# Kernel optimization log

Hardware: AMD Instinct MI355X
Metric: run time of the kernel (lower is better)

The kernel has to match this reference:

```python
import jax, jax.numpy as jnp
import numpy as np

N_NODES = 50000
N_EDGES = 262144
HID = 256
N_CLS = 2


def setup_inputs() -> dict:
    key = jax.random.key(0)
    ks = jax.random.split(key, 6)
    node_repr = jax.random.normal(ks[0], (N_NODES, HID), dtype=jnp.float32)
    src = jax.random.randint(ks[1], (N_EDGES,), 0, N_NODES, dtype=jnp.int64)
    dst = jax.random.randint(ks[2], (N_EDGES,), 0, N_NODES, dtype=jnp.int64)
    # Linear weights stored as (in, out); init ~ torch default scale
    W1 = jax.random.normal(ks[3], (4 * HID, 2 * HID), dtype=jnp.float32) * (1.0 / np.sqrt(4 * HID))
    b1 = jnp.zeros((2 * HID,), dtype=jnp.float32)
    W2 = jax.random.normal(ks[4], (2 * HID, N_CLS), dtype=jnp.float32) * (1.0 / np.sqrt(2 * HID))
    b2 = jnp.zeros((N_CLS,), dtype=jnp.float32)
    return {"node_repr": node_repr, "src": src, "dst": dst,
            "W1": W1, "b1": b1, "W2": W2, "b2": b2}


def reference(node_repr, src, dst, W1, b1, W2, b2):
    h_i = node_repr[src]                      # [E, H] gather
    h_j = node_repr[dst]                      # [E, H] gather
    edge_input = jnp.concatenate(
        [h_i, h_j, jnp.abs(h_i - h_j), h_i * h_j], axis=1)  # [E, 4H]
    h = jax.nn.relu(edge_input @ W1 + b1)     # [E, 2H]; dropout = identity (eval)
    return h @ W2 + b2                        # [E, C]
```

## Files before the change

### kernel.cpp

```cpp
#include <hip/hip_runtime.h>

#define N_NODES 50000
#define E_EDGES 262144

typedef __attribute__((ext_vector_type(8))) _Float16 f16x8;
typedef __attribute__((ext_vector_type(2))) _Float16 f16x2;
typedef __attribute__((ext_vector_type(4))) float f32x4;

union V16 { uint4 u; f16x8 h; };
union U32 { unsigned u; f16x2 p; };

__device__ __forceinline__ unsigned h2pack(float a, float b) {
  union { _Float16 h[2]; unsigned u; } r;
  r.h[0] = (_Float16)a;
  r.h[1] = (_Float16)b;
  return r.u;
}
__device__ __forceinline__ void async_gather16(const void* gptr, void* lptr) {
  __builtin_amdgcn_global_load_lds(
      (const __attribute__((address_space(1))) void*)gptr,
      (__attribute__((address_space(3))) void*)lptr, 16, 0, 0);
}

__global__ __launch_bounds__(256) void prep_all_kernel(
    const float* __restrict__ node, const float* __restrict__ w1,
    unsigned short* __restrict__ nodeb, unsigned short* __restrict__ w1pp2) {
  const int bx = blockIdx.x;
  if (bx < 6250) {
    int i = (bx * 256 + threadIdx.x) * 8;
    float4 f0 = *(const float4*)(node + i);
    float4 f1 = *(const float4*)(node + i + 4);
    uint4 o;
    o.x = h2pack(f0.x, f0.y);
    o.y = h2pack(f0.z, f0.w);
    o.z = h2pack(f1.x, f1.y);
    o.w = h2pack(f1.z, f1.w);
    *(uint4*)(nodeb + i) = o;
  } else {
    int t = (bx - 6250) * 256 + threadIdx.x;
    int step = t >> 13;
    int rem = t & 8191;
    int sq = rem >> 9;
    int col = rem & 511;
    int s = sq >> 2, qd = sq & 3;
    int k0 = s * 256 + step * 32 + qd * 8;
    float f[8];
#pragma unroll
    for (int i = 0; i < 8; ++i) f[i] = w1[(size_t)(k0 + i) * 512 + col];
    uint4 o;
    o.x = h2pack(f[0], f[1]);
    o.y = h2pack(f[2], f[3]);
    o.z = h2pack(f[4], f[5]);
    o.w = h2pack(f[6], f[7]);
    *(uint4*)(w1pp2 + (size_t)t * 8) = o;
  }
}

__global__ __launch_bounds__(512) void edge_mlp_kernel(
    const unsigned short* __restrict__ nodeb,
    const unsigned short* __restrict__ w1pp2,
    const int* __restrict__ src,
    const int* __restrict__ dst,
    const float* __restrict__ b1,
    const float* __restrict__ w2,
    const float* __restrict__ b2,
    float* __restrict__ out) {
  __shared__ char smem[65536];

  const int tid = threadIdx.x;
  const int wid = tid >> 6;
  const int lane = tid & 63;
  const int quad = lane >> 4;
  const int l16 = lane & 15;
  const int bx = blockIdx.x;
  const int xc = bx & 7;
  const int m_idx = (bx >> 3) * 8 + xc;
  const int row0 = m_idx * 64;
  const int n0 = wid * 64;

  const char* nodeB = (const char*)nodeb;
  const char* w1B = (const char*)w1pp2;

  const unsigned bQ = (unsigned)(quad * 8192 + (n0 + l16) * 16);
  const char* w1s = w1B;

  const unsigned aXor = (unsigned)(l16 & 7);
  const unsigned aBase = (unsigned)(l16 * 512);

  f32x4 acc[4][4];
#pragma unroll
  for (int mt = 0; mt < 4; ++mt)
#pragma unroll
    for (int nt = 0; nt < 4; ++nt)
      acc[mt][nt] = (f32x4){0.f, 0.f, 0.f, 0.f};

  {
    const int eh = tid >> 5;
    const unsigned wsw = (unsigned)(((tid & 31) ^ (eh & 7)) << 4);
#pragma unroll
    for (int c = 0; c < 4; ++c) {
      int e = c * 16 + eh;
      unsigned so = ((unsigned)src[row0 + e] << 9) + wsw;
      unsigned do_ = ((unsigned)dst[row0 + e] << 9) + wsw;
      async_gather16(nodeB + so, smem + c * 8192 + wid * 1024);
      async_gather16(nodeB + do_, smem + 32768 + c * 8192 + wid * 1024);
    }
  }
  __syncthreads();

#pragma unroll 2
  for (int step = 0; step < 8; ++step) {
    V16 bf[4][4];
#pragma unroll
    for (int s = 0; s < 4; ++s)
#pragma unroll
      for (int nt = 0; nt < 4; ++nt)
        bf[s][nt].u = *(const uint4*)(w1s + (bQ + (unsigned)(s * 32768 + nt * 256)));
    const unsigned stq = (unsigned)(step * 4 + quad);
    V16 hi[4], hj[4];
#pragma unroll
    for (int mt = 0; mt < 4; ++mt) {
      unsigned ao = (unsigned)(mt * 16 * 512) + aBase + ((stq ^ aXor) << 4);
      hi[mt].u = *(const uint4*)(smem + ao);
      hj[mt].u = *(const uint4*)(smem + 32768 + ao);
    }
#pragma unroll
    for (int mt = 0; mt < 4; ++mt)
#pragma unroll
      for (int nt = 0; nt < 4; ++nt)
        acc[mt][nt] = __builtin_amdgcn_mfma_f32_16x16x32_f16(hi[mt].h, bf[0][nt].h, acc[mt][nt], 0, 0, 0);
#pragma unroll
    for (int mt = 0; mt < 4; ++mt)
#pragma unroll
      for (int nt = 0; nt < 4; ++nt)
        acc[mt][nt] = __builtin_amdgcn_mfma_f32_16x16x32_f16(hj[mt].h, bf[1][nt].h, acc[mt][nt], 0, 0, 0);
#pragma unroll
    for (int mt = 0; mt < 4; ++mt) {
      const unsigned hw[4] = {hi[mt].u.x, hi[mt].u.y, hi[mt].u.z, hi[mt].u.w};
      const unsigned jw[4] = {hj[mt].u.x, hj[mt].u.y, hj[mt].u.z, hj[mt].u.w};
      unsigned d[4], pr[4];
#pragma unroll
      for (int w = 0; w < 4; ++w) {
        U32 hx, jx, dd, pp;
        hx.u = hw[w];
        jx.u = jw[w];
        dd.p = hx.p - jx.p;
        d[w] = dd.u & 0x7fff7fffu;
        pp.p = hx.p * jx.p;
        pr[w] = pp.u;
      }
      V16 a2, a3;
      a2.u = make_uint4(d[0], d[1], d[2], d[3]);
      a3.u = make_uint4(pr[0], pr[1], pr[2], pr[3]);
#pragma unroll
      for (int nt = 0; nt < 4; ++nt)
        acc[mt][nt] = __builtin_amdgcn_mfma_f32_16x16x32_f16(a2.h, bf[2][nt].h, acc[mt][nt], 0, 0, 0);
#pragma unroll
      for (int nt = 0; nt < 4; ++nt)
        acc[mt][nt] = __builtin_amdgcn_mfma_f32_16x16x32_f16(a3.h, bf[3][nt].h, acc[mt][nt], 0, 0, 0);
    }
    w1s += 131072;
  }

  float* red = (float*)smem;
  __syncthreads();
#pragma unroll
  for (int mt = 0; mt < 4; ++mt) {
    float pc0[4] = {0.f, 0.f, 0.f, 0.f};
    float pc1[4] = {0.f, 0.f, 0.f, 0.f};
#pragma unroll
    for (int nt = 0; nt < 4; ++nt) {
      int gc = n0 + nt * 16 + l16;
      float b1v = b1[gc];
      float w20 = w2[gc * 2 + 0];
      float w21 = w2[gc * 2 + 1];
#pragma unroll
      for (int r = 0; r < 4; ++r) {
        float v = fmaxf(acc[mt][nt][r] + b1v, 0.f);
        pc0[r] = fmaf(v, w20, pc0[r]);
        pc1[r] = fmaf(v, w21, pc1[r]);
      }
    }
#pragma unroll
    for (int r = 0; r < 4; ++r) {
      float s0 = pc0[r], s1 = pc1[r];
#pragma unroll
      for (int off = 1; off < 16; off <<= 1) {
        s0 += __shfl_xor(s0, off);
        s1 += __shfl_xor(s1, off);
      }
      int el = mt * 16 + quad * 4 + r;
      if (l16 == 0) red[wid * 128 + el * 2 + 0] = s0;
      if (l16 == 1) red[wid * 128 + el * 2 + 1] = s1;
    }
  }
  __syncthreads();
  if (tid < 128) {
    float s = b2[tid & 1];
#pragma unroll
    for (int w = 0; w < 8; ++w) s += red[w * 128 + tid];
    out[(size_t)row0 * 2 + tid] = s;
  }
}

extern "C" void kernel_launch(void* const* d_in, const int* in_sizes, int n_in,
                              void* d_out, int out_size, void* d_ws, size_t ws_size,
                              hipStream_t stream) {
  const float* node = (const float*)d_in[0];
  const int* src = (const int*)d_in[1];
  const int* dst = (const int*)d_in[2];
  const float* W1 = (const float*)d_in[3];
  const float* b1 = (const float*)d_in[4];
  const float* W2 = (const float*)d_in[5];
  const float* b2 = (const float*)d_in[6];
  float* out = (float*)d_out;

  unsigned short* nodeb = (unsigned short*)d_ws;
  unsigned short* w1pp2 = (unsigned short*)((char*)d_ws + 25600000);

  prep_all_kernel<<<6506, 256, 0, stream>>>(node, W1, nodeb, w1pp2);
  edge_mlp_kernel<<<4096, 512, 0, stream>>>(nodeb, w1pp2, src, dst, b1, W2, b2, out);
}
```

Before: 411.2 us.

## Switch edge MLP GEMM to 32x32x16 MFMA tiles with matching LDS swizzle

Replaces the 16x16x32 f16 MFMA tiling (4x4 accumulators per wave) with 32x32x16 MFMA (2x2 accumulators of 16 floats). The LDS gather swizzle, A/B fragment addressing and epilogue reduction are reworked to match the new lane-to-row mapping. The aim is fewer MFMA issues and fewer fragment loads per unit of work, since larger MFMA tiles reuse operands more. In exchange the epilogue needs a 32-lane shuffle reduction, and the larger per-lane output fragments may change register pressure.

Result: faster. 401.8 us (median of 2 runs) (-2.3%).

```diff
diff --git a/kernel.cpp b/kernel.cpp
--- a/kernel.cpp
+++ b/kernel.cpp
@@ -5,7 +5,7 @@
 
 typedef __attribute__((ext_vector_type(8))) _Float16 f16x8;
 typedef __attribute__((ext_vector_type(2))) _Float16 f16x2;
-typedef __attribute__((ext_vector_type(4))) float f32x4;
+typedef __attribute__((ext_vector_type(16))) float f32x16;
 
 union V16 { uint4 u; f16x8 h; };
 union U32 { unsigned u; f16x2 p; };
@@ -70,8 +70,8 @@
   const int tid = threadIdx.x;
   const int wid = tid >> 6;
   const int lane = tid & 63;
-  const int quad = lane >> 4;
-  const int l16 = lane & 15;
+  const int l32 = lane & 31;
+  const int khalf = lane >> 5;
   const int bx = blockIdx.x;
   const int xc = bx & 7;
   const int m_idx = (bx >> 3) * 8 + xc;
@@ -81,25 +81,28 @@
   const char* nodeB = (const char*)nodeb;
   const char* w1B = (const char*)w1pp2;
 
-  const unsigned bQ = (unsigned)(quad * 8192 + (n0 + l16) * 16);
+  const unsigned bQ = (unsigned)(khalf * 8192 + (n0 + l32) * 16);
   const char* w1s = w1B;
 
-  const unsigned aXor = (unsigned)(l16 & 7);
-  const unsigned aBase = (unsigned)(l16 * 512);
-
-  f32x4 acc[4][4];
-#pragma unroll
-  for (int mt = 0; mt < 4; ++mt)
-#pragma unroll
-    for (int nt = 0; nt < 4; ++nt)
-      acc[mt][nt] = (f32x4){0.f, 0.f, 0.f, 0.f};
+  const unsigned aXor = (unsigned)l32;
+  const unsigned aBase = (unsigned)(l32 * 512);
+
+  f32x16 acc[2][2];
+#pragma unroll
+  for (int mt2 = 0; mt2 < 2; ++mt2)
+#pragma unroll
+    for (int nt2 = 0; nt2 < 2; ++nt2)
+#pragma unroll
+      for (int r = 0; r < 16; ++r)
+        acc[mt2][nt2][r] = 0.f;
 
   {
     const int eh = tid >> 5;
-    const unsigned wsw = (unsigned)(((tid & 31) ^ (eh & 7)) << 4);
 #pragma unroll
     for (int c = 0; c < 4; ++c) {
       int e = c * 16 + eh;
+      unsigned xv = (unsigned)((((c & 1) << 4) | eh));
+      unsigned wsw = (((unsigned)(tid & 31)) ^ xv) << 4;
       unsigned so = ((unsigned)src[row0 + e] << 9) + wsw;
       unsigned do_ = ((unsigned)dst[row0 + e] << 9) + wsw;
       async_gather16(nodeB + so, smem + c * 8192 + wid * 1024);
@@ -110,88 +113,102 @@
 
 #pragma unroll 2
   for (int step = 0; step < 8; ++step) {
-    V16 bf[4][4];
+    V16 bf[4][2][2];
 #pragma unroll
     for (int s = 0; s < 4; ++s)
 #pragma unroll
-      for (int nt = 0; nt < 4; ++nt)
-        bf[s][nt].u = *(const uint4*)(w1s + (bQ + (unsigned)(s * 32768 + nt * 256)));
-    const unsigned stq = (unsigned)(step * 4 + quad);
-    V16 hi[4], hj[4];
-#pragma unroll
-    for (int mt = 0; mt < 4; ++mt) {
-      unsigned ao = (unsigned)(mt * 16 * 512) + aBase + ((stq ^ aXor) << 4);
-      hi[mt].u = *(const uint4*)(smem + ao);
-      hj[mt].u = *(const uint4*)(smem + 32768 + ao);
-    }
-#pragma unroll
-    for (int mt = 0; mt < 4; ++mt)
-#pragma unroll
-      for (int nt = 0; nt < 4; ++nt)
-        acc[mt][nt] = __builtin_amdgcn_mfma_f32_16x16x32_f16(hi[mt].h, bf[0][nt].h, acc[mt][nt], 0, 0, 0);
-#pragma unroll
-    for (int mt = 0; mt < 4; ++mt)
-#pragma unroll
-      for (int nt = 0; nt < 4; ++nt)
-        acc[mt][nt] = __builtin_amdgcn_mfma_f32_16x16x32_f16(hj[mt].h, bf[1][nt].h, acc[mt][nt], 0, 0, 0);
-#pragma unroll
-    for (int mt = 0; mt < 4; ++mt) {
-      const unsigned hw[4] = {hi[mt].u.x, hi[mt].u.y, hi[mt].u.z, hi[mt].u.w};
-      const unsigned jw[4] = {hj[mt].u.x, hj[mt].u.y, hj[mt].u.z, hj[mt].u.w};
-      unsigned d[4], pr[4];
-#pragma unroll
-      for (int w = 0; w < 4; ++w) {
-        U32 hx, jx, dd, pp;
-        hx.u = hw[w];
-        jx.u = jw[w];
-        dd.p = hx.p - jx.p;
-        d[w] = dd.u & 0x7fff7fffu;
-        pp.p = hx.p * jx.p;
-        pr[w] = pp.u;
-      }
-      V16 a2, a3;
-      a2.u = make_uint4(d[0], d[1], d[2], d[3]);
-      a3.u = make_uint4(pr[0], pr[1], pr[2], pr[3]);
-#pragma unroll
-      for (int nt = 0; nt < 4; ++nt)
-        acc[mt][nt] = __builtin_amdgcn_mfma_f32_16x16x32_f16(a2.h, bf[2][nt].h, acc[mt][nt], 0, 0, 0);
-#pragma unroll
-      for (int nt = 0; nt < 4; ++nt)
-        acc[mt][nt] = __builtin_amdgcn_mfma_f32_16x16x32_f16(a3.h, bf[3][nt].h, acc[mt][nt], 0, 0, 0);
-    }
+      for (int sl = 0; sl < 2; ++sl)
+#pragma unroll
+        for (int nt2 = 0; nt2 < 2; ++nt2)
+          bf[s][sl][nt2].u = *(const uint4*)(
+              w1s + (bQ + (unsigned)(s * 32768 + sl * 16384 + nt2 * 512)));
+    V16 hi[2][2], hj[2][2];
+#pragma unroll
+    for (int mt2 = 0; mt2 < 2; ++mt2)
+#pragma unroll
+      for (int sl = 0; sl < 2; ++sl) {
+        unsigned u = (unsigned)(step * 4 + sl * 2 + khalf);
+        unsigned ao = (unsigned)(mt2 * 16384) + aBase + ((u ^ aXor) << 4);
+        hi[mt2][sl].u = *(const uint4*)(smem + ao);
+        hj[mt2][sl].u = *(const uint4*)(smem + 32768 + ao);
+      }
+#pragma unroll
+    for (int mt2 = 0; mt2 < 2; ++mt2)
+#pragma unroll
+      for (int sl = 0; sl < 2; ++sl)
+#pragma unroll
+        for (int nt2 = 0; nt2 < 2; ++nt2)
+          acc[mt2][nt2] = __builtin_amdgcn_mfma_f32_32x32x16_f16(
+              hi[mt2][sl].h, bf[0][sl][nt2].h, acc[mt2][nt2], 0, 0, 0);
+#pragma unroll
+    for (int mt2 = 0; mt2 < 2; ++mt2)
+#pragma unroll
+      for (int sl = 0; sl < 2; ++sl)
+#pragma unroll
+        for (int nt2 = 0; nt2 < 2; ++nt2)
+          acc[mt2][nt2] = __builtin_amdgcn_mfma_f32_32x32x16_f16(
+              hj[mt2][sl].h, bf[1][sl][nt2].h, acc[mt2][nt2], 0, 0, 0);
+#pragma unroll
+    for (int mt2 = 0; mt2 < 2; ++mt2)
+#pragma unroll
+      for (int sl = 0; sl < 2; ++sl) {
+        const unsigned hw[4] = {hi[mt2][sl].u.x, hi[mt2][sl].u.y, hi[mt2][sl].u.z, hi[mt2][sl].u.w};
+        const unsigned jw[4] = {hj[mt2][sl].u.x, hj[mt2][sl].u.y, hj[mt2][sl].u.z, hj[mt2][sl].u.w};
+        unsigned d[4], pr[4];
+#pragma unroll
+        for (int w = 0; w < 4; ++w) {
+          U32 hx, jx, dd, pp;
+          hx.u = hw[w];
+          jx.u = jw[w];
+          dd.p = hx.p - jx.p;
+          d[w] = dd.u & 0x7fff7fffu;
+          pp.p = hx.p * jx.p;
+          pr[w] = pp.u;
+        }
+        V16 a2, a3;
+        a2.u = make_uint4(d[0], d[1], d[2], d[3]);
+        a3.u = make_uint4(pr[0], pr[1], pr[2], pr[3]);
+#pragma unroll
+        for (int nt2 = 0; nt2 < 2; ++nt2)
+          acc[mt2][nt2] = __builtin_amdgcn_mfma_f32_32x32x16_f16(
+              a2.h, bf[2][sl][nt2].h, acc[mt2][nt2], 0, 0, 0);
+#pragma unroll
+        for (int nt2 = 0; nt2 < 2; ++nt2)
+          acc[mt2][nt2] = __builtin_amdgcn_mfma_f32_32x32x16_f16(
+              a3.h, bf[3][sl][nt2].h, acc[mt2][nt2], 0, 0, 0);
+      }
     w1s += 131072;
   }
 
   float* red = (float*)smem;
   __syncthreads();
-#pragma unroll
-  for (int mt = 0; mt < 4; ++mt) {
-    float pc0[4] = {0.f, 0.f, 0.f, 0.f};
-    float pc1[4] = {0.f, 0.f, 0.f, 0.f};
-#pragma unroll
-    for (int nt = 0; nt < 4; ++nt) {
-      int gc = n0 + nt * 16 + l16;
-      float b1v = b1[gc];
-      float w20 = w2[gc * 2 + 0];
-      float w21 = w2[gc * 2 + 1];
-#pragma unroll
-      for (int r = 0; r < 4; ++r) {
-        float v = fmaxf(acc[mt][nt][r] + b1v, 0.f);
-        pc0[r] = fmaf(v, w20, pc0[r]);
-        pc1[r] = fmaf(v, w21, pc1[r]);
-      }
-    }
-#pragma unroll
-    for (int r = 0; r < 4; ++r) {
-      float s0 = pc0[r], s1 = pc1[r];
-#pragma unroll
-      for (int off = 1; off < 16; off <<= 1) {
-        s0 += __shfl_xor(s0, off);
-        s1 += __shfl_xor(s1, off);
-      }
-      int el = mt * 16 + quad * 4 + r;
-      if (l16 == 0) red[wid * 128 + el * 2 + 0] = s0;
-      if (l16 == 1) red[wid * 128 + el * 2 + 1] = s1;
+  float b1v[2], w20[2], w21[2];
+#pragma unroll
+  for (int nt2 = 0; nt2 < 2; ++nt2) {
+    int gc = n0 + nt2 * 32 + l32;
+    b1v[nt2] = b1[gc];
+    w20[nt2] = w2[gc * 2 + 0];
+    w21[nt2] = w2[gc * 2 + 1];
+  }
+#pragma unroll
+  for (int mt2 = 0; mt2 < 2; ++mt2) {
+#pragma unroll
+    for (int r = 0; r < 16; ++r) {
+      float pc0 = 0.f, pc1 = 0.f;
+#pragma unroll
+      for (int nt2 = 0; nt2 < 2; ++nt2) {
+        float v = fmaxf(acc[mt2][nt2][r] + b1v[nt2], 0.f);
+        pc0 = fmaf(v, w20[nt2], pc0);
+        pc1 = fmaf(v, w21[nt2], pc1);
+      }
+#pragma unroll
+      for (int off = 1; off < 32; off <<= 1) {
+        pc0 += __shfl_xor(pc0, off);
+        pc1 += __shfl_xor(pc1, off);
+      }
+      int el = mt2 * 32 + (r & 3) + 8 * (r >> 2) + 4 * khalf;
+      if (l32 == 0) red[wid * 128 + el * 2 + 0] = pc0;
+      if (l32 == 1) red[wid * 128 + el * 2 + 1] = pc1;
     }
   }
   __syncthreads();
```
